# Optimization experiments

Measured on AMD Instinct MI355X. Metric: run time of the kernel, lower is better.

Reference implementation:

```python
import jax, jax.numpy as jnp
import numpy as np

EPS = 1e-5  # torch group_norm default
GROUPS = 32


def _nin(t, W, b):
    # torch Nin: einsum('bchw,co->bowh') transposes spatial dims, then adds bias
    return jnp.einsum('bchw,co->bowh', t, W) + b


def setup_inputs() -> dict:
    key = jax.random.key(0)
    ks = jax.random.split(key, 9)
    B, C, N = 16, 512, 32
    x = jax.random.normal(ks[0], (B, C, N, N), jnp.float32)
    sc = 0.02
    Wq = jax.random.normal(ks[1], (C, C), jnp.float32) * sc
    Wk = jax.random.normal(ks[2], (C, C), jnp.float32) * sc
    Wv = jax.random.normal(ks[3], (C, C), jnp.float32) * sc
    Wn = jax.random.normal(ks[4], (C, C), jnp.float32) * sc
    bq = jnp.zeros((1, C, 1, 1), jnp.float32)
    bk = jnp.zeros((1, C, 1, 1), jnp.float32)
    bv = jnp.zeros((1, C, 1, 1), jnp.float32)
    bn = jnp.zeros((1, C, 1, 1), jnp.float32)
    return {"x": x, "Wq": Wq, "bq": bq, "Wk": Wk, "bk": bk,
            "Wv": Wv, "bv": bv, "Wn": Wn, "bn": bn}


def reference(x, Wq, bq, Wk, bk, Wv, bv, Wn, bn):
    B, C, H, W = x.shape
    # GroupNorm(32) with no affine params
    xg = x.reshape(B, GROUPS, -1)
    mu = xg.mean(-1, keepdims=True)
    var = xg.var(-1, keepdims=True)
    h = ((xg - mu) / jnp.sqrt(var + EPS)).reshape(B, C, H, W)
    # Nin projections -> spatially transposed (B, C, W, H)
    q = _nin(h, Wq, bq)
    k = _nin(h, Wk, bk)
    v = _nin(h, Wv, bv)
    # scores s[b,w1,w2,h1,h2] = sum_c q[b,c,w1,h1] k[b,c,w2,h2] * C^-0.5
    s = jnp.einsum('bcwh,bcWH->bwWhH', q, k) * (C ** -0.5)
    # softmax over flat (h1,h2) blocks exactly as the torch reshape does
    s = jax.nn.softmax(s.reshape(B, H, W, H * W), axis=-1).reshape(B, H, W, H, W)
    # torch.einsum('bHWHW, bcWH -> bcWH', w, v) takes the DIAGONAL over the
    # repeated H and W labels: diag[b,i,j] = s[b,i,j,i,j], then elementwise
    # scales v: out[b,c,w,h] = diag[b,h,w] * v[b,c,w,h]
    i = jnp.arange(H)
    j = jnp.arange(W)
    diag = s[:, i[:, None], j[None, :], i[:, None], j[None, :]]  # (B,H,W)
    h2 = v * jnp.swapaxes(diag, 1, 2)[:, None]  # (B,C,W,H)
    out = _nin(h2, Wn, bn)  # transposes back -> (B,C,H,W)
    return x + out
```

## Files before the change

### kernel.cpp

```cpp
#include <hip/hip_runtime.h>
#include <hip/hip_bf16.h>

typedef __attribute__((ext_vector_type(8))) short short8;
typedef __attribute__((ext_vector_type(4))) float floatx4;

#define MFMA16(a, b, c) __builtin_amdgcn_mfma_f32_16x16x32_bf16((a), (b), (c), 0, 0, 0)

__device__ __forceinline__ short f2bf(float f) {
    union { float f; unsigned u; } x; x.f = f;
    unsigned r = (x.u + 0x7fffu + ((x.u >> 16) & 1u)) >> 16;
    return (short)r;
}

__device__ __forceinline__ void gl2lds16(const short* g, short* l) {
    void* gv = const_cast<short*>(g);
    __builtin_amdgcn_global_load_lds((__attribute__((address_space(1))) void*)gv,
                                     (__attribute__((address_space(3))) void*)l,
                                     16, 0, 0);
}

__global__ void transpose_w4(const float* __restrict__ Wq, const float* __restrict__ Wk,
                             const float* __restrict__ Wv, const float* __restrict__ Wn,
                             const float* __restrict__ bq, const float* __restrict__ bk,
                             const float* __restrict__ bv,
                             short* __restrict__ Wqkv_t, short* __restrict__ Wn_t,
                             float* __restrict__ bias_cat) {
    __shared__ float t[32][33];
    int z = blockIdx.z;
    const float* Wsrc = (z == 0) ? Wq : (z == 1) ? Wk : (z == 2) ? Wv : Wn;
    int o0 = blockIdx.x * 32, c0 = blockIdx.y * 32;
    int lx = threadIdx.x, ly = threadIdx.y;
    for (int i = ly; i < 32; i += 8) t[i][lx] = Wsrc[(size_t)(c0 + i) * 512 + o0 + lx];
    __syncthreads();
    for (int i = ly; i < 32; i += 8) {
        short v = f2bf(t[lx][i]);
        if (z < 3) Wqkv_t[(size_t)(z * 512 + o0 + i) * 512 + c0 + lx] = v;
        else       Wn_t[(size_t)(o0 + i) * 512 + c0 + lx] = v;
    }
    if (z < 3 && blockIdx.y == 0 && ly == 0) {
        const float* bsrc = (z == 0) ? bq : (z == 1) ? bk : bv;
        bias_cat[z * 512 + o0 + lx] = bsrc[o0 + lx];
    }
}

__global__ __launch_bounds__(256) void groupnorm_k(const float* __restrict__ x,
                                                   short* __restrict__ hnt) {
    int b = blockIdx.x >> 5, g = blockIdx.x & 31;
    const float* xg = x + ((size_t)b * 512 + g * 16) * 1024;
    const float4* xg4 = (const float4*)xg;
    float s = 0.f, ss = 0.f;
    for (int i = threadIdx.x; i < 4096; i += 256) {
        float4 v = xg4[i];
        s  += v.x + v.y + v.z + v.w;
        ss += v.x * v.x + v.y * v.y + v.z * v.z + v.w * v.w;
    }
#pragma unroll
    for (int off = 32; off > 0; off >>= 1) {
        s  += __shfl_down(s,  off, 64);
        ss += __shfl_down(ss, off, 64);
    }
    __shared__ float red[8];
    int w = threadIdx.x >> 6;
    if ((threadIdx.x & 63) == 0) { red[w] = s; red[4 + w] = ss; }
    __syncthreads();
    float S  = red[0] + red[1] + red[2] + red[3];
    float SS = red[4] + red[5] + red[6] + red[7];
    float mean = S * (1.f / 16384.f);
    float var  = SS * (1.f / 16384.f) - mean * mean;
    float rstd = rsqrtf(var + 1e-5f);
    __shared__ __attribute__((aligned(16))) short tile[16 * 1026];
    for (int i = threadIdx.x; i < 4096; i += 256) {
        float4 v = xg4[i];
        int c = i >> 8, p = (i & 255) * 4;
        short* tp = tile + c * 1026 + p;
        tp[0] = f2bf((v.x - mean) * rstd);
        tp[1] = f2bf((v.y - mean) * rstd);
        tp[2] = f2bf((v.z - mean) * rstd);
        tp[3] = f2bf((v.w - mean) * rstd);
    }
    __syncthreads();
    for (int i = threadIdx.x; i < 2048; i += 256) {
        int p = i >> 1, half = i & 1;
        short8 v;
#pragma unroll
        for (int j = 0; j < 8; ++j) v[j] = tile[(half * 8 + j) * 1026 + p];
        *(short8*)(hnt + ((size_t)b * 1024 + p) * 512 + g * 16 + half * 8) = v;
    }
}

__global__ __launch_bounds__(256) void qkv_gemm(const short* __restrict__ A,
                                                const short* __restrict__ Wt,
                                                const float* __restrict__ bias_cat,
                                                short* __restrict__ Qp,
                                                short* __restrict__ Kp,
                                                short* __restrict__ Vb) {
    const int tid = threadIdx.x;
    const int wv = tid >> 6, ln = tid & 63;
    const int m0 = blockIdx.x * 128, n0 = blockIdx.y * 128;
    const size_t BS = 1024 * 512;
    const short* Ab = A + (size_t)blockIdx.z * BS;
    const int tsel = n0 >> 9;
    const int permute = (tsel < 2);
    short* Ob = ((tsel == 0) ? Qp : (tsel == 1) ? Kp : Vb) + (size_t)blockIdx.z * BS;

    __shared__ __attribute__((aligned(16))) short As[2][128 * 32];
    __shared__ __attribute__((aligned(16))) short Bs[2][128 * 32];

    floatx4 acc[4][4] = {};
    const int wm = (wv >> 1) * 64, wn = (wv & 1) * 64;
    const int fr = ln & 15, fq = ln >> 4;

    int sr[2], sq[2];
#pragma unroll
    for (int j = 0; j < 2; ++j) {
        int s = (wv * 2 + j) * 64 + ln;
        sr[j] = s >> 2;
        sq[j] = ((s & 3) ^ ((sr[j] >> 1) & 3)) * 8;
    }

#pragma unroll
    for (int j = 0; j < 2; ++j) {
        gl2lds16(Ab + (size_t)(m0 + sr[j]) * 512 + sq[j], &As[0][(wv * 2 + j) * 512]);
        gl2lds16(Wt + (size_t)(n0 + sr[j]) * 512 + sq[j], &Bs[0][(wv * 2 + j) * 512]);
    }
    __syncthreads();

    int cur = 0;
    for (int kk = 0; kk < 512; kk += 32) {
        if (kk < 480) {
            int nxt = cur ^ 1;
#pragma unroll
            for (int j = 0; j < 2; ++j) {
                gl2lds16(Ab + (size_t)(m0 + sr[j]) * 512 + kk + 32 + sq[j], &As[nxt][(wv * 2 + j) * 512]);
                gl2lds16(Wt + (size_t)(n0 + sr[j]) * 512 + kk + 32 + sq[j], &Bs[nxt][(wv * 2 + j) * 512]);
            }
        }
        short8 af[4], bfr[4];
#pragma unroll
        for (int t = 0; t < 4; ++t) {
            int ra = wm + t * 16 + fr;
            af[t]  = *(const short8*)(&As[cur][ra * 32 + ((fq ^ ((ra >> 1) & 3)) * 8)]);
            int rb = wn + t * 16 + fr;
            bfr[t] = *(const short8*)(&Bs[cur][rb * 32 + ((fq ^ ((rb >> 1) & 3)) * 8)]);
        }
#pragma unroll
        for (int mt = 0; mt < 4; ++mt)
#pragma unroll
            for (int nt = 0; nt < 4; ++nt)
                acc[mt][nt] = MFMA16(af[mt], bfr[nt], acc[mt][nt]);
        __syncthreads();
        cur ^= 1;
    }
#pragma unroll
    for (int mt = 0; mt < 4; ++mt) {
#pragma unroll
        for (int nt = 0; nt < 4; ++nt) {
            int n = n0 + wn + nt * 16 + fr;
            float bvv = bias_cat[n];
            int nn = n & 511;
#pragma unroll
            for (int r = 0; r < 4; ++r) {
                int m = m0 + wm + mt * 16 + fq * 4 + r;
                int mrow = permute ? ((m & 31) * 32 + (m >> 5)) : m;
                Ob[(size_t)mrow * 512 + nn] = f2bf(acc[mt][nt][r] + bvv);
            }
        }
    }
}

__global__ __launch_bounds__(256, 2) void attn_sm(const short* __restrict__ Qp,
                                                  const short* __restrict__ Kp,
                                                  float* __restrict__ Dm) {
    const int tid = threadIdx.x;
    const int wv = tid >> 6, ln = tid & 63;
    const int m0 = blockIdx.x * 128, n0 = blockIdx.y * 256, b = blockIdx.z;
    const short* Qb = Qp + (size_t)b * (1024 * 512);
    const short* Kb = Kp + (size_t)b * (1024 * 512);

    __shared__ __attribute__((aligned(16))) short As[2][128 * 32];
    __shared__ __attribute__((aligned(16))) short Bs[2][256 * 32];

    floatx4 acc[4][8] = {};
    const int wm = (wv >> 1) * 64, wn = (wv & 1) * 128;
    const int fr = ln & 15, fq = ln >> 4;

    int ar[2], aq[2], br[4], bq_[4];
#pragma unroll
    for (int j = 0; j < 2; ++j) {
        int s = (wv * 2 + j) * 64 + ln;
        ar[j] = s >> 2;
        aq[j] = ((s & 3) ^ ((ar[j] >> 1) & 3)) * 8;
    }
#pragma unroll
    for (int j = 0; j < 4; ++j) {
        int s = (wv * 4 + j) * 64 + ln;
        br[j] = s >> 2;
        bq_[j] = ((s & 3) ^ ((br[j] >> 1) & 3)) * 8;
    }

#pragma unroll
    for (int j = 0; j < 2; ++j)
        gl2lds16(Qb + (size_t)(m0 + ar[j]) * 512 + aq[j], &As[0][(wv * 2 + j) * 512]);
#pragma unroll
    for (int j = 0; j < 4; ++j)
        gl2lds16(Kb + (size_t)(n0 + br[j]) * 512 + bq_[j], &Bs[0][(wv * 4 + j) * 512]);
    __syncthreads();

    int cur = 0;
    for (int kk = 0; kk < 512; kk += 32) {
        if (kk < 480) {
            int nxt = cur ^ 1;
#pragma unroll
            for (int j = 0; j < 2; ++j)
                gl2lds16(Qb + (size_t)(m0 + ar[j]) * 512 + kk + 32 + aq[j], &As[nxt][(wv * 2 + j) * 512]);
#pragma unroll
            for (int j = 0; j < 4; ++j)
                gl2lds16(Kb + (size_t)(n0 + br[j]) * 512 + kk + 32 + bq_[j], &Bs[nxt][(wv * 4 + j) * 512]);
        }
        short8 af[4], bfr[8];
#pragma unroll
        for (int t = 0; t < 4; ++t) {
            int ra = wm + t * 16 + fr;
            af[t] = *(const short8*)(&As[cur][ra * 32 + ((fq ^ ((ra >> 1) & 3)) * 8)]);
        }
#pragma unroll
        for (int u = 0; u < 8; ++u) {
            int rb = wn + u * 16 + fr;
            bfr[u] = *(const short8*)(&Bs[cur][rb * 32 + ((fq ^ ((rb >> 1) & 3)) * 8)]);
        }
#pragma unroll
        for (int mt = 0; mt < 4; ++mt)
#pragma unroll
            for (int nt = 0; nt < 8; ++nt)
                acc[mt][nt] = MFMA16(af[mt], bfr[nt], acc[mt][nt]);
        __syncthreads();
        cur ^= 1;
    }

    const float scale = 0.04419417382415922f;
    const int wbase = (m0 + wm) >> 5;
    const int Wbase = (n0 + wn) >> 5;
#pragma unroll
    for (int si = 0; si < 2; ++si) {
#pragma unroll
        for (int sj = 0; sj < 4; ++sj) {
            int wg = wbase + si, Wg = Wbase + sj;
            float tv[16];
            float mx = -3.0e38f;
#pragma unroll
            for (int mi = 0; mi < 2; ++mi)
#pragma unroll
                for (int ni = 0; ni < 2; ++ni)
#pragma unroll
                    for (int r = 0; r < 4; ++r) {
                        float u = acc[2 * si + mi][2 * sj + ni][r] * scale;
                        tv[(mi * 2 + ni) * 4 + r] = u;
                        mx = fmaxf(mx, u);
                    }
#pragma unroll
            for (int off = 32; off > 0; off >>= 1) mx = fmaxf(mx, __shfl_xor(mx, off, 64));
            float se = 0.f;
#pragma unroll
            for (int i = 0; i < 16; ++i) se += __expf(tv[i] - mx);
#pragma unroll
            for (int off = 32; off > 0; off >>= 1) se += __shfl_xor(se, off, 64);
            if (fq == ((wg >> 2) & 3) && fr == (Wg & 15)) {
                int mi = wg >> 4, ni = Wg >> 4;
                float numer = tv[(mi * 2 + ni) * 4 + (wg & 3)];
                Dm[((size_t)b * 32 + wg) * 32 + Wg] = __expf(numer - mx) / se;
            }
        }
    }
}

__global__ __launch_bounds__(256) void out_gemm(const short* __restrict__ A,
                                                const short* __restrict__ Wt,
                                                const float* __restrict__ Dm,
                                                const float* __restrict__ bnb,
                                                const float* __restrict__ x,
                                                float* __restrict__ out) {
    const int tid = threadIdx.x;
    const int wv = tid >> 6, ln = tid & 63;
    const int m0 = blockIdx.x * 128, n0 = blockIdx.y * 128, b = blockIdx.z;
    const size_t BS = 1024 * 512;
    const short* Ab = A + (size_t)b * BS;

    __shared__ __attribute__((aligned(16))) short As[2][128 * 32];
    __shared__ __attribute__((aligned(16))) short Bs[2][128 * 32];

    floatx4 acc[4][4] = {};
    const int wm = (wv >> 1) * 64, wn = (wv & 1) * 64;
    const int fr = ln & 15, fq = ln >> 4;

    int sr[2], sq[2];
#pragma unroll
    for (int j = 0; j < 2; ++j) {
        int s = (wv * 2 + j) * 64 + ln;
        sr[j] = s >> 2;
        sq[j] = ((s & 3) ^ ((sr[j] >> 1) & 3)) * 8;
    }

#pragma unroll
    for (int j = 0; j < 2; ++j) {
        gl2lds16(Ab + (size_t)(m0 + sr[j]) * 512 + sq[j], &As[0][(wv * 2 + j) * 512]);
        gl2lds16(Wt + (size_t)(n0 + sr[j]) * 512 + sq[j], &Bs[0][(wv * 2 + j) * 512]);
    }
    __syncthreads();

    int cur = 0;
    for (int kk = 0; kk < 512; kk += 32) {
        if (kk < 480) {
            int nxt = cur ^ 1;
#pragma unroll
            for (int j = 0; j < 2; ++j) {
                gl2lds16(Ab + (size_t)(m0 + sr[j]) * 512 + kk + 32 + sq[j], &As[nxt][(wv * 2 + j) * 512]);
                gl2lds16(Wt + (size_t)(n0 + sr[j]) * 512 + kk + 32 + sq[j], &Bs[nxt][(wv * 2 + j) * 512]);
            }
        }
        short8 af[4], bfr[4];
#pragma unroll
        for (int t = 0; t < 4; ++t) {
            int ra = wm + t * 16 + fr;
            af[t]  = *(const short8*)(&As[cur][ra * 32 + ((fq ^ ((ra >> 1) & 3)) * 8)]);
            int rb = wn + t * 16 + fr;
            bfr[t] = *(const short8*)(&Bs[cur][rb * 32 + ((fq ^ ((rb >> 1) & 3)) * 8)]);
        }
#pragma unroll
        for (int mt = 0; mt < 4; ++mt)
#pragma unroll
            for (int nt = 0; nt < 4; ++nt)
                acc[mt][nt] = MFMA16(af[mt], bfr[nt], acc[mt][nt]);
        __syncthreads();
        cur ^= 1;
    }
#pragma unroll
    for (int mt = 0; mt < 4; ++mt) {
        int mbase = m0 + wm + mt * 16 + fq * 4;
        float4 d4 = *(const float4*)(Dm + (size_t)b * 1024 + mbase);
#pragma unroll
        for (int nt = 0; nt < 4; ++nt) {
            int n = n0 + wn + nt * 16 + fr;
            float bvv = bnb[n];
            size_t base = ((size_t)b * 512 + n) * 1024 + mbase;
            float4 x4 = *(const float4*)(x + base);
            float4 o;
            o.x = x4.x + d4.x * acc[mt][nt][0] + bvv;
            o.y = x4.y + d4.y * acc[mt][nt][1] + bvv;
            o.z = x4.z + d4.z * acc[mt][nt][2] + bvv;
            o.w = x4.w + d4.w * acc[mt][nt][3] + bvv;
            *(float4*)(out + base) = o;
        }
    }
}

extern "C" void kernel_launch(void* const* d_in, const int* in_sizes, int n_in,
                              void* d_out, int out_size, void* d_ws, size_t ws_size,
                              hipStream_t stream) {
    const float* x  = (const float*)d_in[0];
    const float* Wq = (const float*)d_in[1];
    const float* bq = (const float*)d_in[2];
    const float* Wk = (const float*)d_in[3];
    const float* bk = (const float*)d_in[4];
    const float* Wv = (const float*)d_in[5];
    const float* bv = (const float*)d_in[6];
    const float* Wn = (const float*)d_in[7];
    const float* bn = (const float*)d_in[8];
    float* out = (float*)d_out;
    char* ws = (char*)d_ws;

    const size_t WQKV = (size_t)1536 * 512 * 2;
    const size_t WSZ  = (size_t)512 * 512 * 2;
    const size_t BIAS = 1536 * sizeof(float);
    const size_t TSZ  = (size_t)16 * 1024 * 512 * 2;
    short* Wqkv_t   = (short*)(ws);
    short* Wn_t     = (short*)(ws + WQKV);
    float* bias_cat = (float*)(ws + WQKV + WSZ);
    char*  base     = ws + WQKV + WSZ + BIAS;
    short* hnt = (short*)(base);
    short* Qp  = (short*)(base + TSZ);
    short* Kp  = (short*)(base + 2 * TSZ);
    short* Vb  = (short*)(base + 3 * TSZ);
    float* Dm  = (float*)(base + 4 * TSZ);

    transpose_w4<<<dim3(16, 16, 4), dim3(32, 8), 0, stream>>>(
        Wq, Wk, Wv, Wn, bq, bk, bv, Wqkv_t, Wn_t, bias_cat);
    groupnorm_k<<<512, 256, 0, stream>>>(x, hnt);
    qkv_gemm<<<dim3(8, 12, 16), 256, 0, stream>>>(hnt, Wqkv_t, bias_cat, Qp, Kp, Vb);
    attn_sm<<<dim3(8, 4, 16), 256, 0, stream>>>(Qp, Kp, Dm);
    out_gemm<<<dim3(8, 4, 16), 256, 0, stream>>>(Vb, Wn_t, Dm, bn, x, out);
}
```

Baseline: 210.7 us.

## Triple-buffer LDS tiles with partial vmcnt waits in all three GEMM kernels

Replaces the double-buffered K loop in the QKV, attention-score and output GEMMs with a three-stage LDS ring. Two tiles are prefetched up front, and each iteration waits with s_waitcnt vmcnt only for the oldest outstanding tile rather than draining all loads. The aim is to keep more global-to-LDS traffic in flight behind the MFMA work. In exchange it uses more shared memory per block, which may lower occupancy, especially for attn_sm with its 256-wide B tile, and it depends on getting the vmcnt counts right.

```diff
diff --git a/kernel.cpp b/kernel.cpp
--- a/kernel.cpp
+++ b/kernel.cpp
@@ -5,6 +5,8 @@
 typedef __attribute__((ext_vector_type(4))) float floatx4;
 
 #define MFMA16(a, b, c) __builtin_amdgcn_mfma_f32_16x16x32_bf16((a), (b), (c), 0, 0, 0)
+#define WAIT_VM(N) asm volatile("s_waitcnt vmcnt(" #N ")" ::: "memory")
+#define BAR() __builtin_amdgcn_s_barrier()
 
 __device__ __forceinline__ short f2bf(float f) {
     union { float f; unsigned u; } x; x.f = f;
@@ -103,8 +105,8 @@
     const int permute = (tsel < 2);
     short* Ob = ((tsel == 0) ? Qp : (tsel == 1) ? Kp : Vb) + (size_t)blockIdx.z * BS;
 
-    __shared__ __attribute__((aligned(16))) short As[2][128 * 32];
-    __shared__ __attribute__((aligned(16))) short Bs[2][128 * 32];
+    __shared__ __attribute__((aligned(16))) short As[3][128 * 32];
+    __shared__ __attribute__((aligned(16))) short Bs[3][128 * 32];
 
     floatx4 acc[4][4] = {};
     const int wm = (wv >> 1) * 64, wn = (wv & 1) * 64;
@@ -118,39 +120,52 @@
         sq[j] = ((s & 3) ^ ((sr[j] >> 1) & 3)) * 8;
     }
 
-#pragma unroll
-    for (int j = 0; j < 2; ++j) {
-        gl2lds16(Ab + (size_t)(m0 + sr[j]) * 512 + sq[j], &As[0][(wv * 2 + j) * 512]);
-        gl2lds16(Wt + (size_t)(n0 + sr[j]) * 512 + sq[j], &Bs[0][(wv * 2 + j) * 512]);
-    }
-    __syncthreads();
-
-    int cur = 0;
-    for (int kk = 0; kk < 512; kk += 32) {
-        if (kk < 480) {
-            int nxt = cur ^ 1;
-#pragma unroll
-            for (int j = 0; j < 2; ++j) {
-                gl2lds16(Ab + (size_t)(m0 + sr[j]) * 512 + kk + 32 + sq[j], &As[nxt][(wv * 2 + j) * 512]);
-                gl2lds16(Wt + (size_t)(n0 + sr[j]) * 512 + kk + 32 + sq[j], &Bs[nxt][(wv * 2 + j) * 512]);
-            }
-        }
+    short* a0 = &As[0][0]; short* a1 = &As[1][0]; short* a2 = &As[2][0];
+    short* b0 = &Bs[0][0]; short* b1 = &Bs[1][0]; short* b2 = &Bs[2][0];
+
+#pragma unroll
+    for (int j = 0; j < 2; ++j) {
+        gl2lds16(Ab + (size_t)(m0 + sr[j]) * 512 + sq[j],      a0 + (wv * 2 + j) * 512);
+        gl2lds16(Wt + (size_t)(n0 + sr[j]) * 512 + sq[j],      b0 + (wv * 2 + j) * 512);
+        gl2lds16(Ab + (size_t)(m0 + sr[j]) * 512 + 32 + sq[j], a1 + (wv * 2 + j) * 512);
+        gl2lds16(Wt + (size_t)(n0 + sr[j]) * 512 + 32 + sq[j], b1 + (wv * 2 + j) * 512);
+    }
+
+    auto compute = [&](const short* Ap, const short* Bp) {
         short8 af[4], bfr[4];
 #pragma unroll
         for (int t = 0; t < 4; ++t) {
             int ra = wm + t * 16 + fr;
-            af[t]  = *(const short8*)(&As[cur][ra * 32 + ((fq ^ ((ra >> 1) & 3)) * 8)]);
+            af[t]  = *(const short8*)(Ap + ra * 32 + ((fq ^ ((ra >> 1) & 3)) * 8));
             int rb = wn + t * 16 + fr;
-            bfr[t] = *(const short8*)(&Bs[cur][rb * 32 + ((fq ^ ((rb >> 1) & 3)) * 8)]);
+            bfr[t] = *(const short8*)(Bp + rb * 32 + ((fq ^ ((rb >> 1) & 3)) * 8));
         }
 #pragma unroll
         for (int mt = 0; mt < 4; ++mt)
 #pragma unroll
             for (int nt = 0; nt < 4; ++nt)
                 acc[mt][nt] = MFMA16(af[mt], bfr[nt], acc[mt][nt]);
-        __syncthreads();
-        cur ^= 1;
-    }
+    };
+
+    for (int t = 0; t < 14; ++t) {
+        int kp = t * 32 + 64;
+#pragma unroll
+        for (int j = 0; j < 2; ++j) {
+            gl2lds16(Ab + (size_t)(m0 + sr[j]) * 512 + kp + sq[j], a2 + (wv * 2 + j) * 512);
+            gl2lds16(Wt + (size_t)(n0 + sr[j]) * 512 + kp + sq[j], b2 + (wv * 2 + j) * 512);
+        }
+        WAIT_VM(8);
+        BAR();
+        compute(a0, b0);
+        BAR();
+        short* ta = a0; a0 = a1; a1 = a2; a2 = ta;
+        short* tb = b0; b0 = b1; b1 = b2; b2 = tb;
+    }
+    WAIT_VM(4); BAR();
+    compute(a0, b0);
+    WAIT_VM(0); BAR();
+    compute(a1, b1);
+
 #pragma unroll
     for (int mt = 0; mt < 4; ++mt) {
 #pragma unroll
@@ -177,8 +192,8 @@
     const short* Qb = Qp + (size_t)b * (1024 * 512);
     const short* Kb = Kp + (size_t)b * (1024 * 512);
 
-    __shared__ __attribute__((aligned(16))) short As[2][128 * 32];
-    __shared__ __attribute__((aligned(16))) short Bs[2][256 * 32];
+    __shared__ __attribute__((aligned(16))) short As[3][128 * 32];
+    __shared__ __attribute__((aligned(16))) short Bs[3][256 * 32];
 
     floatx4 acc[4][8] = {};
     const int wm = (wv >> 1) * 64, wn = (wv & 1) * 128;
@@ -198,44 +213,58 @@
         bq_[j] = ((s & 3) ^ ((br[j] >> 1) & 3)) * 8;
     }
 
-#pragma unroll
-    for (int j = 0; j < 2; ++j)
-        gl2lds16(Qb + (size_t)(m0 + ar[j]) * 512 + aq[j], &As[0][(wv * 2 + j) * 512]);
-#pragma unroll
-    for (int j = 0; j < 4; ++j)
-        gl2lds16(Kb + (size_t)(n0 + br[j]) * 512 + bq_[j], &Bs[0][(wv * 4 + j) * 512]);
-    __syncthreads();
-
-    int cur = 0;
-    for (int kk = 0; kk < 512; kk += 32) {
-        if (kk < 480) {
-            int nxt = cur ^ 1;
-#pragma unroll
-            for (int j = 0; j < 2; ++j)
-                gl2lds16(Qb + (size_t)(m0 + ar[j]) * 512 + kk + 32 + aq[j], &As[nxt][(wv * 2 + j) * 512]);
-#pragma unroll
-            for (int j = 0; j < 4; ++j)
-                gl2lds16(Kb + (size_t)(n0 + br[j]) * 512 + kk + 32 + bq_[j], &Bs[nxt][(wv * 4 + j) * 512]);
-        }
+    short* a0 = &As[0][0]; short* a1 = &As[1][0]; short* a2 = &As[2][0];
+    short* b0 = &Bs[0][0]; short* b1 = &Bs[1][0]; short* b2 = &Bs[2][0];
+
+#pragma unroll
+    for (int j = 0; j < 2; ++j) {
+        gl2lds16(Qb + (size_t)(m0 + ar[j]) * 512 + aq[j],      a0 + (wv * 2 + j) * 512);
+        gl2lds16(Qb + (size_t)(m0 + ar[j]) * 512 + 32 + aq[j], a1 + (wv * 2 + j) * 512);
+    }
+#pragma unroll
+    for (int j = 0; j < 4; ++j) {
+        gl2lds16(Kb + (size_t)(n0 + br[j]) * 512 + bq_[j],      b0 + (wv * 4 + j) * 512);
+        gl2lds16(Kb + (size_t)(n0 + br[j]) * 512 + 32 + bq_[j], b1 + (wv * 4 + j) * 512);
+    }
+
+    auto compute = [&](const short* Ap, const short* Bp) {
         short8 af[4], bfr[8];
 #pragma unroll
         for (int t = 0; t < 4; ++t) {
             int ra = wm + t * 16 + fr;
-            af[t] = *(const short8*)(&As[cur][ra * 32 + ((fq ^ ((ra >> 1) & 3)) * 8)]);
+            af[t] = *(const short8*)(Ap + ra * 32 + ((fq ^ ((ra >> 1) & 3)) * 8));
         }
 #pragma unroll
         for (int u = 0; u < 8; ++u) {
             int rb = wn + u * 16 + fr;
-            bfr[u] = *(const short8*)(&Bs[cur][rb * 32 + ((fq ^ ((rb >> 1) & 3)) * 8)]);
+            bfr[u] = *(const short8*)(Bp + rb * 32 + ((fq ^ ((rb >> 1) & 3)) * 8));
         }
 #pragma unroll
         for (int mt = 0; mt < 4; ++mt)
 #pragma unroll
             for (int nt = 0; nt < 8; ++nt)
                 acc[mt][nt] = MFMA16(af[mt], bfr[nt], acc[mt][nt]);
-        __syncthreads();
-        cur ^= 1;
-    }
+    };
+
+    for (int t = 0; t < 14; ++t) {
+        int kp = t * 32 + 64;
+#pragma unroll
+        for (int j = 0; j < 2; ++j)
+            gl2lds16(Qb + (size_t)(m0 + ar[j]) * 512 + kp + aq[j], a2 + (wv * 2 + j) * 512);
+#pragma unroll
+        for (int j = 0; j < 4; ++j)
+            gl2lds16(Kb + (size_t)(n0 + br[j]) * 512 + kp + bq_[j], b2 + (wv * 4 + j) * 512);
+        WAIT_VM(12);
+        BAR();
+        compute(a0, b0);
+        BAR();
+        short* ta = a0; a0 = a1; a1 = a2; a2 = ta;
+        short* tb = b0; b0 = b1; b1 = b2; b2 = tb;
+    }
+    WAIT_VM(6); BAR();
+    compute(a0, b0);
+    WAIT_VM(0); BAR();
+    compute(a1, b1);
 
     const float scale = 0.04419417382415922f;
     const int wbase = (m0 + wm) >> 5;
@@ -285,8 +314,8 @@
     const size_t BS = 1024 * 512;
     const short* Ab = A + (size_t)b * BS;
 
-    __shared__ __attribute__((aligned(16))) short As[2][128 * 32];
-    __shared__ __attribute__((aligned(16))) short Bs[2][128 * 32];
+    __shared__ __attribute__((aligned(16))) short As[3][128 * 32];
+    __shared__ __attribute__((aligned(16))) short Bs[3][128 * 32];
 
     floatx4 acc[4][4] = {};
     const int wm = (wv >> 1) * 64, wn = (wv & 1) * 64;
@@ -300,39 +329,52 @@
         sq[j] = ((s & 3) ^ ((sr[j] >> 1) & 3)) * 8;
     }
 
-#pragma unroll
-    for (int j = 0; j < 2; ++j) {
-        gl2lds16(Ab + (size_t)(m0 + sr[j]) * 512 + sq[j], &As[0][(wv * 2 + j) * 512]);
-        gl2lds16(Wt + (size_t)(n0 + sr[j]) * 512 + sq[j], &Bs[0][(wv * 2 + j) * 512]);
-    }
-    __syncthreads();
-
-    int cur = 0;
-    for (int kk = 0; kk < 512; kk += 32) {
-        if (kk < 480) {
-            int nxt = cur ^ 1;
-#pragma unroll
-            for (int j = 0; j < 2; ++j) {
-                gl2lds16(Ab + (size_t)(m0 + sr[j]) * 512 + kk + 32 + sq[j], &As[nxt][(wv * 2 + j) * 512]);
-                gl2lds16(Wt + (size_t)(n0 + sr[j]) * 512 + kk + 32 + sq[j], &Bs[nxt][(wv * 2 + j) * 512]);
-            }
-        }
+    short* a0 = &As[0][0]; short* a1 = &As[1][0]; short* a2 = &As[2][0];
+    short* b0 = &Bs[0][0]; short* b1 = &Bs[1][0]; short* b2 = &Bs[2][0];
+
+#pragma unroll
+    for (int j = 0; j < 2; ++j) {
+        gl2lds16(Ab + (size_t)(m0 + sr[j]) * 512 + sq[j],      a0 + (wv * 2 + j) * 512);
+        gl2lds16(Wt + (size_t)(n0 + sr[j]) * 512 + sq[j],      b0 + (wv * 2 + j) * 512);
+        gl2lds16(Ab + (size_t)(m0 + sr[j]) * 512 + 32 + sq[j], a1 + (wv * 2 + j) * 512);
+        gl2lds16(Wt + (size_t)(n0 + sr[j]) * 512 + 32 + sq[j], b1 + (wv * 2 + j) * 512);
+    }
+
+    auto compute = [&](const short* Ap, const short* Bp) {
         short8 af[4], bfr[4];
 #pragma unroll
         for (int t = 0; t < 4; ++t) {
             int ra = wm + t * 16 + fr;
-            af[t]  = *(const short8*)(&As[cur][ra * 32 + ((fq ^ ((ra >> 1) & 3)) * 8)]);
+            af[t]  = *(const short8*)(Ap + ra * 32 + ((fq ^ ((ra >> 1) & 3)) * 8));
             int rb = wn + t * 16 + fr;
-            bfr[t] = *(const short8*)(&Bs[cur][rb * 32 + ((fq ^ ((rb >> 1) & 3)) * 8)]);
+            bfr[t] = *(const short8*)(Bp + rb * 32 + ((fq ^ ((rb >> 1) & 3)) * 8));
         }
 #pragma unroll
         for (int mt = 0; mt < 4; ++mt)
 #pragma unroll
             for (int nt = 0; nt < 4; ++nt)
                 acc[mt][nt] = MFMA16(af[mt], bfr[nt], acc[mt][nt]);
-        __syncthreads();
-        cur ^= 1;
-    }
+    };
+
+    for (int t = 0; t < 14; ++t) {
+        int kp = t * 32 + 64;
+#pragma unroll
+        for (int j = 0; j < 2; ++j) {
+            gl2lds16(Ab + (size_t)(m0 + sr[j]) * 512 + kp + sq[j], a2 + (wv * 2 + j) * 512);
+            gl2lds16(Wt + (size_t)(n0 + sr[j]) * 512 + kp + sq[j], b2 + (wv * 2 + j) * 512);
+        }
+        WAIT_VM(8);
+        BAR();
+        compute(a0, b0);
+        BAR();
+        short* ta = a0; a0 = a1; a1 = a2; a2 = ta;
+        short* tb = b0; b0 = b1; b1 = b2; b2 = tb;
+    }
+    WAIT_VM(4); BAR();
+    compute(a0, b0);
+    WAIT_VM(0); BAR();
+    compute(a1, b1);
+
 #pragma unroll
     for (int mt = 0; mt < 4; ++mt) {
         int mbase = m0 + wm + mt * 16 + fq * 4;
```

After: 211.2 us. No clear change (+0.2%).
